# Kernel tuning notes

Hardware: AMD Instinct MI355X
Metric: run time of the kernel (lower is better)

Reference implementation:

```python
import jax, jax.numpy as jnp
import numpy as np

B, L, NV = 16, 512, 321
D, PL, ST = 128, 16, 8
P = (L - PL) // ST + 2  # 64 patches (replication pad of `stride` on the right)
E, K, H = 8, 2, 512     # experts, top-n gates, expert hidden (4*d_model)
PRED = 96
BAL_COEF, Z_COEF = 0.01, 0.001


def sinusoidal_pe(n, d):
    pos = np.arange(n)[:, None].astype(np.float32)
    div = np.exp(np.arange(0, d, 2).astype(np.float32) * -(np.log(10000.0) / d))
    pe = np.zeros((n, d), dtype=np.float32)
    pe[:, 0::2] = np.sin(pos * div)
    pe[:, 1::2] = np.cos(pos * div)
    return jnp.asarray(pe)


def setup_inputs() -> dict:
    key = jax.random.key(0)
    ks = jax.random.split(key, 12)
    s = lambda i, shape, sc: jax.random.normal(ks[i], shape, jnp.float32) * sc
    return {
        "x_enc": jax.random.normal(ks[0], (B, L, NV), jnp.float32),
        "x_mark_enc": jax.random.normal(ks[1], (B, L, 4), jnp.float32),
        "x_dec": jax.random.normal(ks[2], (B, PRED, NV), jnp.float32),
        "x_mark_dec": jax.random.normal(ks[3], (B, PRED, 4), jnp.float32),
        "W_val": s(4, (PL, D), PL ** -0.5),
        "W_g": s(5, (D, E), D ** -0.5),
        "W1": s(6, (E, D, H), D ** -0.5),
        "b1": jnp.zeros((E, H), jnp.float32),
        "W2": s(7, (E, H, D), H ** -0.5),
        "b2": jnp.zeros((E, D), jnp.float32),
        "W_head": s(8, (D * P, PRED), (D * P) ** -0.5),
        "b_head": jnp.zeros((PRED,), jnp.float32),
    }


def _forward(x_enc, W_val, W_g, W1, b1, W2, b2, W_head, b_head):
    # RevIN-style instance norm (means detached as in torch .detach())
    means = jax.lax.stop_gradient(jnp.mean(x_enc, axis=1, keepdims=True))
    xc = x_enc - means
    stdev = jnp.sqrt(jnp.var(xc, axis=1, keepdims=True) + 1e-5)
    xn = xc / stdev

    # Patch embedding: [B, NV, L] -> replicate-pad -> unfold -> linear + sinusoidal PE
    x = jnp.transpose(xn, (0, 2, 1))                        # [B, NV, L]
    x = jnp.pad(x, ((0, 0), (0, 0), (0, ST)), mode="edge")  # ReplicationPad1d((0, stride))
    idx = np.arange(P)[:, None] * ST + np.arange(PL)        # [P, PL]
    patches = x[:, :, idx]                                  # [B, NV, P, PL]
    tok = patches.reshape(B * NV, P, PL)
    emb = tok @ W_val + sinusoidal_pe(P, D)[None]           # [N, P, D]

    # MoE: top-n softmax gating (gates not renormalized), balance + router-z aux losses
    t = emb.reshape(-1, D)                                  # [T, D], T = B*NV*P
    logits = t @ W_g                                        # [T, E]
    probs = jax.nn.softmax(logits, axis=-1)
    topv, topi = jax.lax.top_k(probs, K)                    # [T, K]

    out = jnp.zeros_like(t)
    for e in range(E):  # fixed small expert count; each expert is a GELU MLP
        h = jax.nn.gelu(t @ W1[e] + b1[e], approximate=False) @ W2[e] + b2[e]
        g = jnp.sum(jnp.where(topi == e, topv, 0.0), axis=-1)  # gate for expert e (0 if unrouted)
        out = out + g[:, None] * h

    me = jnp.mean(probs, axis=0)                                            # mean router prob per expert
    ce = jnp.mean(jax.nn.one_hot(topi, E, dtype=probs.dtype).sum(1), 0) / K  # dispatch fraction per expert
    balance_loss = E * jnp.sum(me * ce)
    z_loss = jnp.mean(jax.nn.logsumexp(logits, axis=-1) ** 2)
    aux = BAL_COEF * balance_loss + Z_COEF * z_loss

    # FlattenHead: [B, NV, P, D] -> [B, NV, D, P] -> flatten(-2) -> Linear(nf, pred_len)
    enc = out.reshape(B, NV, P, D).transpose(0, 1, 3, 2)    # [B, NV, D, P]
    dec = enc.reshape(B, NV, D * P) @ W_head + b_head        # [B, NV, PRED]
    dec = jnp.transpose(dec, (0, 2, 1))                      # [B, PRED, NV]

    # de-normalize
    dec = dec * stdev[:, 0][:, None, :] + means[:, 0][:, None, :]
    return dec, aux


def reference(x_enc, x_mark_enc, x_dec, x_mark_dec, W_val, W_g, W1, b1, W2, b2, W_head, b_head):
    return _forward(x_enc, W_val, W_g, W1, b1, W2, b2, W_head, b_head)
```

## Files before the change

### kernel.cpp

```cpp
#include <hip/hip_runtime.h>
#include <hip/hip_bf16.h>

typedef unsigned short u16;
typedef unsigned int   u32;
typedef unsigned long long u64;
typedef __attribute__((ext_vector_type(8))) short bf16x8;
typedef __attribute__((ext_vector_type(4))) float f32x4;
typedef __attribute__((ext_vector_type(16))) float f32x16;
typedef __attribute__((ext_vector_type(2))) unsigned int u32x2;

#define MFMA16(a,b,c) __builtin_amdgcn_mfma_f32_16x16x32_bf16(a,b,c,0,0,0)
#define MFMA32(a,b,c) __builtin_amdgcn_mfma_f32_32x32x16_bf16(a,b,c,0,0,0)

#define NV_   321
#define B_    16
#define L_    512
#define D_    128
#define P_    64
#define E_    8
#define H_    512
#define NRW   5136
#define NTOK  328704
#define DP_   8192
#define NBUCK 329728

static __device__ __forceinline__ u16 f2bf(float f){
  __hip_bfloat16 h = __float2bfloat16(f);
  return *reinterpret_cast<u16*>(&h);
}

static __device__ __forceinline__ float gelu_f(float x){
  float x2 = x*x;
  float p  = __builtin_fmaf(-0.1029433f, x2, -2.3022083f);
  float a  = x*p;
  float en = exp2f(a);
  float r  = __builtin_amdgcn_rcpf(1.0f + en);
  return x*r;
}

static constexpr size_t alup(size_t x){ return (x + 255) & ~(size_t)255; }
static constexpr size_t OFF_MEAN = 0;
static constexpr size_t OFF_RSTD = OFF_MEAN + alup((size_t)NRW*4);
static constexpr size_t OFF_STD  = OFF_RSTD + alup((size_t)NRW*4);
static constexpr size_t OFF_XT   = OFF_STD  + alup((size_t)NRW*4);
static constexpr size_t OFF_PE   = OFF_XT   + alup((size_t)NRW*L_*4);
static constexpr size_t OFF_W1T  = OFF_PE   + alup((size_t)P_*D_*4);
static constexpr size_t OFF_W2T  = OFF_W1T  + alup((size_t)E_*H_*D_*2);
static constexpr size_t OFF_WHT  = OFF_W2T  + alup((size_t)E_*D_*H_*2);
static constexpr size_t OFF_T    = OFF_WHT  + alup((size_t)96*DP_*2);
static constexpr size_t OFF_TOPI = OFF_T    + alup((size_t)NTOK*D_*2);
static constexpr size_t OFF_GATE = OFF_TOPI + alup((size_t)NTOK*4);
static constexpr size_t OFF_CNTR = OFF_GATE + alup((size_t)NTOK*8);
static constexpr size_t OFF_BTOK = OFF_CNTR + alup((size_t)1024);
static constexpr size_t OFF_BGT  = OFF_BTOK + alup((size_t)2*NBUCK*4);
static constexpr size_t OFF_OUT  = OFF_BGT  + alup((size_t)2*NBUCK*4);
static constexpr size_t OFF_MEAND= OFF_OUT  + alup((size_t)NTOK*D_*2);
static constexpr size_t OFF_RSTDD= OFF_MEAND+ alup((size_t)NRW*8);
static constexpr size_t OFF_WVG  = OFF_RSTDD+ alup((size_t)NRW*8);
static constexpr size_t OFF_PEG  = OFF_WVG  + alup((size_t)16*8*8);
static constexpr size_t OFF_PG   = OFF_PEG  + alup((size_t)P_*E_*8);
static constexpr size_t OFF_PI   = OFF_PG   + alup((size_t)NRW*12*4);



__global__ void k_xt(const float* __restrict__ x, float* __restrict__ xT){
  __shared__ float tile[32][33];
  int b = blockIdx.z;
  int v0 = blockIdx.x*32, l0 = blockIdx.y*32;
  int tx = threadIdx.x, ty = threadIdx.y;
  for(int i=ty;i<32;i+=8){
    int l = l0+i, v = v0+tx;
    tile[i][tx] = (v<NV_) ? x[((size_t)b*L_ + l)*NV_ + v] : 0.f;
  }
  __syncthreads();
  for(int i=ty;i<32;i+=8){
    int v = v0+i, l = l0+tx;
    if(v<NV_) xT[((size_t)(b*NV_+v))*L_ + l] = tile[tx][i];
  }
}

__global__ void k_stats(const float* __restrict__ xT, float* meanp, float* rstdp, float* stdp,
                        double* meand, double* rstdd){
  __shared__ double s1[256], s2[256];
  int r = blockIdx.x, t = threadIdx.x;
  double a = (double)xT[(size_t)r*L_ + t], b = (double)xT[(size_t)r*L_ + 256 + t];
  s1[t]=a+b; s2[t]=a*a+b*b;
  __syncthreads();
  for(int o=128;o>0;o>>=1){ if(t<o){ s1[t]+=s1[t+o]; s2[t]+=s2[t+o]; } __syncthreads(); }
  if(t==0){
    double m = s1[0]*(1.0/512.0);
    double var = s2[0]*(1.0/512.0) - m*m;
    double sd = sqrt(var + 1e-5);
    meanp[r]=(float)m; stdp[r]=(float)sd; rstdp[r]=(float)(1.0/sd);
    meand[r]=m; rstdd[r]=1.0/sd;
  }
}

__global__ void k_prep(const float* __restrict__ Wval, const float* __restrict__ Wg,
                       float* __restrict__ pef, double* __restrict__ Wvg,
                       double* __restrict__ peg){
  int t = threadIdx.x;
  for(int i=t;i<8192;i+=256){
    int p = i>>7, d = i&127, k = d>>1;
    double div = exp(-(double)(2*k) * (9.210340371976184 /128.0));
    double ang = (double)p * div;
    double v = (d&1) ? cos(ang) : sin(ang);
    pef[i] = (float)v;
  }
  __syncthreads();
  if(t<128){
    int j = t>>3, e = t&7;
    double acc = 0.0;
    for(int d=0;d<128;d++) acc += (double)Wval[j*128+d] * (double)Wg[d*8+e];
    Wvg[t] = acc;
  }
  for(int q=t;q<512;q+=256){
    int p = q>>3, e = q&7;
    double acc = 0.0;
    for(int d=0;d<128;d++) acc += (double)pef[p*128+d] * (double)Wg[d*8+e];
    peg[q] = acc;
  }
}

__global__ void k_wt(const float* __restrict__ in, u16* __restrict__ outp, int R, int C){
  __shared__ float tile[32][33];
  int e = blockIdx.z;
  int c0 = blockIdx.x*32, r0 = blockIdx.y*32;
  const float* src = in + (size_t)e*R*C;
  u16* dst = outp + (size_t)e*R*C;
  int tx=threadIdx.x, ty=threadIdx.y;
  for(int i=ty;i<32;i+=8){
    int r=r0+i, c=c0+tx;
    tile[i][tx] = (r<R && c<C) ? src[(size_t)r*C+c] : 0.f;
  }
  __syncthreads();
  for(int i=ty;i<32;i+=8){
    int c=c0+i, r=r0+tx;
    if(c<C && r<R) dst[(size_t)c*R + r] = f2bf(tile[tx][i]);
  }
}

__global__ void k_wh(const float* __restrict__ Wh, u16* __restrict__ WhT2){
  __shared__ float tile[32][33];
  int d0 = blockIdx.x*32, o0 = blockIdx.y*32, p = blockIdx.z;
  int tx = threadIdx.x, ty = threadIdx.y;
  for(int i=ty;i<32;i+=8){
    int r = (d0+i)*64 + p;
    tile[i][tx] = Wh[(size_t)r*96 + o0 + tx];
  }
  __syncthreads();
  for(int i=ty;i<32;i+=8){
    int o = o0+i;
    WhT2[(size_t)o*DP_ + p*128 + d0 + tx] = f2bf(tile[tx][i]);
  }
}

__global__ __launch_bounds__(256) void k_embed(
    const float* __restrict__ xT, const float* __restrict__ meanp, const float* __restrict__ rstdp,
    const float* __restrict__ Wval, const float* __restrict__ pe,
    u16* __restrict__ tglob)
{
  __shared__ __align__(16) float xn[520];
  int r = blockIdx.x, t = threadIdx.x;
  float mean = meanp[r], rstd = rstdp[r];
  float v0 = (xT[(size_t)r*L_ + t]       - mean)*rstd;
  float v1 = (xT[(size_t)r*L_ + 256 + t] - mean)*rstd;
  xn[t] = v0; xn[t+256] = v1;
  if(t==255){
    #pragma unroll
    for(int i=512;i<520;i++) xn[i]=v1;
  }
  int d0 = (t & 63)*2;
  int p0 = t >> 6;
  float2 w[16];
  #pragma unroll
  for(int j=0;j<16;j++) w[j] = *(const float2*)(Wval + j*128 + d0);
  __syncthreads();

  for(int p=p0;p<64;p+=4){
    const float4* xp = (const float4*)(xn + p*8);
    float4 x0=xp[0], x1=xp[1], x2=xp[2], x3=xp[3];
    float xv[16];
    *(float4*)(xv+0)=x0; *(float4*)(xv+4)=x1; *(float4*)(xv+8)=x2; *(float4*)(xv+12)=x3;
    float2 pw = *(const float2*)(pe + p*128 + d0);
    float a0 = pw.x, a1 = pw.y;
    #pragma unroll
    for(int j=0;j<16;j++){ a0 += xv[j]*w[j].x; a1 += xv[j]*w[j].y; }
    u32 packed = (u32)f2bf(a0) | ((u32)f2bf(a1)<<16);
    *(u32*)(tglob + ((size_t)(r*64+p)*128 + d0)) = packed;
  }
}

__global__ __launch_bounds__(256) void k_gate(
    const float* __restrict__ xT, const double* __restrict__ meand, const double* __restrict__ rstdd,
    const double* __restrict__ Wvg, const double* __restrict__ peg,
    int* __restrict__ topip, float2* __restrict__ gatep,
    float* __restrict__ pg, int* __restrict__ pib)
{
  __shared__ double xn[520];
  __shared__ double lgt[64][9];
  int r = blockIdx.x, t = threadIdx.x;
  double m = meand[r], rs = rstdd[r];
  double v0 = ((double)xT[(size_t)r*L_ + t]       - m)*rs;
  double v1 = ((double)xT[(size_t)r*L_ + 256 + t] - m)*rs;
  xn[t]=v0; xn[t+256]=v1;
  if(t==255){
    #pragma unroll
    for(int i=512;i<520;i++) xn[i]=v1;
  }
  __syncthreads();
  for(int q=t;q<512;q+=256){
    int p = q>>3, e = q&7;
    double acc = peg[q];
    #pragma unroll
    for(int j=0;j<16;j++) acc += xn[p*8+j]*Wvg[j*8+e];
    lgt[p][e] = acc;
  }
  __syncthreads();
  if(t<64){
    int token = r*64 + t;
    double l0[8];
    #pragma unroll
    for(int e=0;e<8;e++) l0[e]=lgt[t][e];
    double mx=l0[0];
    #pragma unroll
    for(int e=1;e<8;e++) mx = fmax(mx,l0[e]);
    int i1=0; double b1v=l0[0];
    #pragma unroll
    for(int e=1;e<8;e++) if(l0[e]>b1v){b1v=l0[e]; i1=e;}
    int i2=-1; double b2v=-1e300;
    #pragma unroll
    for(int e=0;e<8;e++) if(e!=i1 && l0[e]>b2v){b2v=l0[e]; i2=e;}
    float pr[8]; float sum=0.f;
    #pragma unroll
    for(int e=0;e<8;e++){ pr[e]=__expf((float)(l0[e]-mx)); sum+=pr[e]; }
    float inv = 1.f/sum;
    #pragma unroll
    for(int e=0;e<8;e++) pr[e]*=inv;
    topip[token] = i1 | (i2<<8);
    gatep[token] = make_float2(pr[i1], pr[i2]);
    float lse = (float)mx + __logf(sum);
    #pragma unroll
    for(int e=0;e<8;e++){
      float v = pr[e];
      for(int o=32;o>0;o>>=1) v += __shfl_down(v,o);
      if(t==0) pg[r*12+e] = v;
    }
    {
      float z = lse*lse;
      for(int o=32;o>0;o>>=1) z += __shfl_down(z,o);
      if(t==0) pg[r*12+8] = z;
    }
    #pragma unroll
    for(int e=0;e<8;e++){
      u64 m1 = __ballot(i1==e);
      u64 m2 = __ballot(i2==e);
      if(t==0){
        pib[r*16+e]   = (int)__popcll(m1);
        pib[r*16+8+e] = (int)__popcll(m2);
      }
    }
  }
}

__global__ __launch_bounds__(256) void k_aux(const float* __restrict__ pg, const int* __restrict__ pib,
                                             int* __restrict__ ci, float* __restrict__ dout){
  __shared__ double sd[256];
  __shared__ int si[256];
  __shared__ double totd[9];
  __shared__ int toti[16];
  int t = threadIdx.x;
  double accd[9]; int acci[16];
  #pragma unroll
  for(int c=0;c<9;c++) accd[c]=0.0;
  #pragma unroll
  for(int c=0;c<16;c++) acci[c]=0;
  for(int r=t;r<NRW;r+=256){
    #pragma unroll
    for(int c=0;c<9;c++) accd[c] += (double)pg[r*12+c];
    #pragma unroll
    for(int c=0;c<16;c++) acci[c] += pib[r*16+c];
  }
  for(int c=0;c<9;c++){
    sd[t]=accd[c]; __syncthreads();
    for(int o=128;o>0;o>>=1){ if(t<o) sd[t]+=sd[t+o]; __syncthreads(); }
    if(t==0) totd[c]=sd[0];
    __syncthreads();
  }
  for(int c=0;c<16;c++){
    si[t]=acci[c]; __syncthreads();
    for(int o=128;o>0;o>>=1){ if(t<o) si[t]+=si[t+o]; __syncthreads(); }
    if(t==0) toti[c]=si[0];
    __syncthreads();
  }
  if(t==0){
    const double invN = 1.0/(double)NTOK;
    double bal = 0.0;
    int es1=0, bs1=0, es2=0, bs2=0;
    for(int e=0;e<8;e++){
      int c1 = toti[e], c2 = toti[8+e];
      bal += (totd[e]*invN) * ((double)(c1+c2) * invN * 0.5);
      ci[32+e]=es1; ci[16+e]=es1; ci[50+e]=bs1;
      ci[41+e]=es2; ci[24+e]=es2; ci[59+e]=bs2;
      es1 += c1; bs1 += (c1+127)>>7;
      es2 += c2; bs2 += (c2+127)>>7;
    }
    ci[40]=es1; ci[58]=bs1;
    ci[49]=es2; ci[67]=bs2;
    dout[493056] = (float)(0.01*8.0*bal + 0.001*(totd[8]*invN));
  }
}

__global__ __launch_bounds__(256) void k_scatter(const int* __restrict__ topip,
    const float2* __restrict__ gatep, int* __restrict__ ci,
    int* __restrict__ btok, float* __restrict__ bgt){
  __shared__ int lc[16]; __shared__ int lb[16];
  int t = threadIdx.x;
  int token = blockIdx.x*256 + t;
  if(t<16) lc[t]=0;
  __syncthreads();
  int ti = topip[token];
  float2 g = gatep[token];
  int e1 = ti & 255, e2 = (ti>>8)&255;
  int r1 = atomicAdd(&lc[e1],1);
  int r2 = atomicAdd(&lc[8+e2],1);
  __syncthreads();
  if(t<8)            lb[t] = atomicAdd(&ci[16+t],   lc[t]);
  else if(t<16)      lb[t] = atomicAdd(&ci[24+t-8], lc[t]);
  __syncthreads();
  int p1 = lb[e1]+r1, p2 = lb[8+e2]+r2;
  btok[p1] = token;         bgt[p1] = g.x;
  btok[NBUCK+p2] = token;   bgt[NBUCK+p2] = g.y;
}

__global__ __launch_bounds__(256,3) void k_expert(
    const u16* __restrict__ tglob,
    const u16* __restrict__ W1T, const u16* __restrict__ W2T,
    const float* __restrict__ b1g, const float* __restrict__ b2g,
    const int* __restrict__ ci,
    const int* __restrict__ btok, const float* __restrict__ bgt,
    u16* __restrict__ outg, int slot)
{
  __shared__ __align__(16) u16 Wb[2][9472];

  int bid = blockIdx.x, t = threadIdx.x;
  int stB = 32 + slot*9, bsB = 50 + slot*9;
  int boff = slot*NBUCK;
  if(bid >= ci[bsB+8]) return;
  int e = 0;
  #pragma unroll
  for(int k2=1;k2<8;k2++) if(bid >= ci[bsB+k2]) e = k2;
  int row0 = ci[stB+e] + (bid - ci[bsB+e])*128;
  int rend = ci[stB+e+1];

  int wid = t>>6, lane = t&63;
  int m = lane&31, hi = lane>>5;
  int rb = wid*32;

  int posA = row0 + rb + m;
  bool valA = posA < rend;
  int tokA  = valA ? btok[boff+posA] : 0;
  float gt  = valA ? bgt[boff+posA]  : 0.f;
  const u16* arow = tglob + (size_t)tokA*128 + hi*8;
  bf16x8 areg[8];
  #pragma unroll
  for(int ks=0;ks<8;ks++) areg[ks] = *(const bf16x8*)(arow + ks*16);

  int hr = t>>3, q = t&7;
  int dr = t>>1, q2 = t&1;

  {
    const u16* s1 = W1T + ((size_t)e*H_ + hr)*128 + q*16;
    u16* d1 = &Wb[0][hr*136 + q*16];
    *(uint4*)(d1)   = *(const uint4*)(s1);
    *(uint4*)(d1+8) = *(const uint4*)(s1+8);
    const u16* s2 = W2T + ((size_t)e*D_ + dr)*H_ + q2*16;
    u16* d2 = &Wb[0][4352 + dr*40 + q2*16];
    *(uint4*)(d2)   = *(const uint4*)(s2);
    *(uint4*)(d2+8) = *(const uint4*)(s2+8);
  }
  __syncthreads();

  f32x16 accO[4];
  #pragma unroll
  for(int nt=0;nt<4;nt++){
    const float* bp2 = b2g + e*D_ + nt*32 + 4*hi;
    #pragma unroll
    for(int qq=0;qq<4;qq++){
      float4 b4 = *(const float4*)(bp2 + 8*qq);
      accO[nt][4*qq+0]=b4.x; accO[nt][4*qq+1]=b4.y;
      accO[nt][4*qq+2]=b4.z; accO[nt][4*qq+3]=b4.w;
    }
  }

  for(int hc=0;hc<16;hc++){
    const u16* W1c = &Wb[hc&1][0];
    const u16* W2c = &Wb[hc&1][4352];
    uint4 l0,l1,l2,l3;
    if(hc<15){
      const u16* s1 = W1T + ((size_t)e*H_ + (hc+1)*32 + hr)*128 + q*16;
      l0 = *(const uint4*)(s1); l1 = *(const uint4*)(s1+8);
      const u16* s2 = W2T + ((size_t)e*D_ + dr)*H_ + (hc+1)*32 + q2*16;
      l2 = *(const uint4*)(s2); l3 = *(const uint4*)(s2+8);
    }
    f32x16 acc1;
    {
      const float* bp1 = b1g + e*H_ + hc*32 + 4*hi;
      #pragma unroll
      for(int qq=0;qq<4;qq++){
        float4 b4 = *(const float4*)(bp1 + 8*qq);
        acc1[4*qq+0]=b4.x; acc1[4*qq+1]=b4.y;
        acc1[4*qq+2]=b4.z; acc1[4*qq+3]=b4.w;
      }
    }
    #pragma unroll
    for(int ks=0;ks<8;ks++){
      bf16x8 wa = *(const bf16x8*)(W1c + m*136 + ks*16 + hi*8);
      acc1 = MFMA32(wa, areg[ks], acc1);
    }
    u32 pk[8];
    #pragma unroll
    for(int i=0;i<8;i++){
      float g0 = gelu_f(acc1[2*i]);
      float g1 = gelu_f(acc1[2*i+1]);
      asm("v_cvt_pk_bf16_f32 %0, %1, %2" : "=v"(pk[i]) : "v"(g0), "v"(g1));
    }
    union { bf16x8 v; u32 w[4]; } bA, bB;
    u32x2 s02 = __builtin_amdgcn_permlane32_swap(pk[0], pk[2], false, false);
    u32x2 s13 = __builtin_amdgcn_permlane32_swap(pk[1], pk[3], false, false);
    u32x2 s46 = __builtin_amdgcn_permlane32_swap(pk[4], pk[6], false, false);
    u32x2 s57 = __builtin_amdgcn_permlane32_swap(pk[5], pk[7], false, false);
    bA.w[0]=s02.x; bA.w[1]=s13.x; bA.w[2]=s02.y; bA.w[3]=s13.y;
    bB.w[0]=s46.x; bB.w[1]=s57.x; bB.w[2]=s46.y; bB.w[3]=s57.y;
    #pragma unroll
    for(int nt=0;nt<4;nt++){
      bf16x8 a2 = *(const bf16x8*)(W2c + (nt*32+m)*40 + hi*8);
      accO[nt] = MFMA32(a2, bA.v, accO[nt]);
    }
    #pragma unroll
    for(int nt=0;nt<4;nt++){
      bf16x8 a2 = *(const bf16x8*)(W2c + (nt*32+m)*40 + 16 + hi*8);
      accO[nt] = MFMA32(a2, bB.v, accO[nt]);
    }
    if(hc<15){
      u16* d1 = &Wb[(hc+1)&1][hr*136 + q*16];
      *(uint4*)(d1)   = l0; *(uint4*)(d1+8) = l1;
      u16* d2 = &Wb[(hc+1)&1][4352 + dr*40 + q2*16];
      *(uint4*)(d2)   = l2; *(uint4*)(d2+8) = l3;
      __syncthreads();
    }
  }

  if(valA){
    u16* obase = outg + (size_t)tokA*128 + 4*hi;
    #pragma unroll
    for(int nt=0;nt<4;nt++){
      #pragma unroll
      for(int qq=0;qq<4;qq++){
        float v0 = accO[nt][4*qq+0]*gt;
        float v1 = accO[nt][4*qq+1]*gt;
        float v2 = accO[nt][4*qq+2]*gt;
        float v3 = accO[nt][4*qq+3]*gt;
        u32* dp = (u32*)(obase + nt*32 + 8*qq);
        if(slot==1){
          u32x2 old = *(const u32x2*)dp;
          v0 += __uint_as_float(old.x<<16);
          v1 += __uint_as_float(old.x & 0xffff0000u);
          v2 += __uint_as_float(old.y<<16);
          v3 += __uint_as_float(old.y & 0xffff0000u);
        }
        u32 w0, w1;
        asm("v_cvt_pk_bf16_f32 %0, %1, %2" : "=v"(w0) : "v"(v0), "v"(v1));
        asm("v_cvt_pk_bf16_f32 %0, %1, %2" : "=v"(w1) : "v"(v2), "v"(v3));
        u32x2 nv; nv.x = w0; nv.y = w1;
        *(u32x2*)dp = nv;
      }
    }
  }
}

__global__ __launch_bounds__(256) void k_head(const u16* __restrict__ Aout,
    const u16* __restrict__ WhT2, float* __restrict__ dec8){
  int bid = blockIdx.x;
  int mb = bid>>3, kseg = bid&7;
  int t = threadIdx.x, wid = t>>6, lane = t&63;
  int quad = lane>>4, li = lane&15;
  int r0 = mb*64 + wid*16;
  int rowA = r0 + li; if(rowA >= NRW) rowA = NRW-1;
  const u16* aptr = Aout + (size_t)rowA*DP_ + kseg*1024 + quad*8;
  const u16* bptr = WhT2 + (size_t)li*DP_  + kseg*1024 + quad*8;
  f32x4 acc[6];
  #pragma unroll
  for(int j=0;j<6;j++) acc[j]=(f32x4){0,0,0,0};
  #pragma unroll 4
  for(int ks=0;ks<32;ks++){
    bf16x8 af = *(const bf16x8*)(aptr + ks*32);
    #pragma unroll
    for(int nt=0;nt<6;nt++){
      bf16x8 bw = *(const bf16x8*)(bptr + (size_t)nt*16*DP_ + ks*32);
      acc[nt] = MFMA16(af, bw, acc[nt]);
    }
  }
  float* dst = dec8 + (size_t)kseg*NRW*96;
  #pragma unroll
  for(int nt=0;nt<6;nt++)
    #pragma unroll
    for(int rg=0;rg<4;rg++){
      int mm = r0 + quad*4 + rg;
      if(mm < NRW) dst[(size_t)mm*96 + nt*16 + li] = acc[nt][rg];
    }
}

__global__ void k_final(const float* __restrict__ dec8, const float* __restrict__ bhead,
    const float* __restrict__ stdp, const float* __restrict__ meanp, float* __restrict__ outp){
  __shared__ float s[64*97];
  int b = blockIdx.y, v0 = blockIdx.x*64;
  int t = threadIdx.x;
  for(int i=t;i<6144;i+=256){
    int vi = i/96, o = i - vi*96;
    int v = v0+vi;
    float acc = 0.f;
    if(v<NV_){
      size_t base = (size_t)(b*NV_+v)*96 + o;
      #pragma unroll
      for(int ks=0;ks<8;ks++) acc += dec8[(size_t)ks*NRW*96 + base];
    }
    s[vi*97+o] = acc;
  }
  __syncthreads();
  for(int i=t;i<6144;i+=256){
    int o = i>>6, vi = i&63;
    int v = v0+vi;
    if(v<NV_){
      int r = b*NV_+v;
      outp[((size_t)b*96 + o)*NV_ + v] = (s[vi*97+o] + bhead[o])*stdp[r] + meanp[r];
    }
  }
}

extern "C" void kernel_launch(void* const* d_in, const int* in_sizes, int n_in,
                              void* d_out, int out_size, void* d_ws, size_t ws_size,
                              hipStream_t stream){
  const float* x_enc = (const float*)d_in[0];
  const float* W_val = (const float*)d_in[4];
  const float* W_g   = (const float*)d_in[5];
  const float* W1    = (const float*)d_in[6];
  const float* b1    = (const float*)d_in[7];
  const float* W2    = (const float*)d_in[8];
  const float* b2    = (const float*)d_in[9];
  const float* W_head= (const float*)d_in[10];
  const float* b_head= (const float*)d_in[11];
  float* outp = (float*)d_out;
  char* ws = (char*)d_ws;

  float* meanp = (float*)(ws+OFF_MEAN);
  float* rstdp = (float*)(ws+OFF_RSTD);
  float* stdp  = (float*)(ws+OFF_STD);
  float* xT    = (float*)(ws+OFF_XT);
  float* pe    = (float*)(ws+OFF_PE);
  u16*   W1T   = (u16*)(ws+OFF_W1T);
  u16*   W2T   = (u16*)(ws+OFF_W2T);
  u16*   WhT2  = (u16*)(ws+OFF_WHT);
  u16*   tglob = (u16*)(ws+OFF_T);
  float* dec8  = (float*)(ws+OFF_T);
  int*   topip = (int*)(ws+OFF_TOPI);
  float2* gatep= (float2*)(ws+OFF_GATE);
  int*   ci    = (int*)(ws+OFF_CNTR+128);
  int*   btok  = (int*)(ws+OFF_BTOK);
  float* bgt   = (float*)(ws+OFF_BGT);
  u16*   outg  = (u16*)(ws+OFF_OUT);
  double* meand= (double*)(ws+OFF_MEAND);
  double* rstdd= (double*)(ws+OFF_RSTDD);
  double* Wvg  = (double*)(ws+OFF_WVG);
  double* peg  = (double*)(ws+OFF_PEG);
  float* pg    = (float*)(ws+OFF_PG);
  int*   pib   = (int*)(ws+OFF_PI);

  hipMemsetAsync(ws+OFF_CNTR, 0, 1024, stream);

  k_xt<<<dim3(11,16,B_), dim3(32,8), 0, stream>>>(x_enc, xT);
  k_stats<<<NRW, 256, 0, stream>>>(xT, meanp, rstdp, stdp, meand, rstdd);
  k_prep<<<1, 256, 0, stream>>>(W_val, W_g, pe, Wvg, peg);
  k_wt<<<dim3(16,4,E_), dim3(32,8), 0, stream>>>(W1, W1T, 128, 512);
  k_wt<<<dim3(4,16,E_), dim3(32,8), 0, stream>>>(W2, W2T, 512, 128);
  k_wh<<<dim3(4,3,64), dim3(32,8), 0, stream>>>(W_head, WhT2);
  k_embed<<<NRW, 256, 0, stream>>>(xT, meanp, rstdp, W_val, pe, tglob);
  k_gate<<<NRW, 256, 0, stream>>>(xT, meand, rstdd, Wvg, peg, topip, gatep, pg, pib);
  k_aux<<<1, 256, 0, stream>>>(pg, pib, ci, outp);
  k_scatter<<<NTOK/256, 256, 0, stream>>>(topip, gatep, ci, btok, bgt);
  k_expert<<<2576, 256, 0, stream>>>(tglob, W1T, W2T, b1, b2, ci, btok, bgt, outg, 0);
  k_expert<<<2576, 256, 0, stream>>>(tglob, W1T, W2T, b1, b2, ci, btok, bgt, outg, 1);
  k_head<<<648, 256, 0, stream>>>(outg, WhT2, dec8);
  k_final<<<dim3(6,B_), 256, 0, stream>>>(dec8, b_head, stdp, meanp, outp);
}
```

Before: 641.0 us.

## Software-pipeline expert MLP: overlap GEMM2 of previous chunk with GEMM1 of current

Restructures the expert FFN loop so the second GEMM for hidden chunk hc-1 is interleaved with the first GEMM for chunk hc, while the GELU/pack of the current chunk runs after the MFMAs. W1 and W2 get separate double-buffered LDS arrays, b1 is staged once into LDS, and s_setprio is raised around the MFMA bursts. The aim is to hide GELU VALU work and LDS latency behind matrix instructions, at the cost of extra LDS, a prologue and epilogue, and more live registers that may pressure occupancy.

Result: no change. 632.6 us (-1.3%).

```diff
diff --git a/kernel.cpp b/kernel.cpp
--- a/kernel.cpp
+++ b/kernel.cpp
@@ -333,6 +333,35 @@
   btok[NBUCK+p2] = token;   bgt[NBUCK+p2] = g.y;
 }
 
+static __device__ __forceinline__ f32x16 acc1_init(const float* b1l, int hc, int hi){
+  f32x16 a;
+  const float* bp = b1l + hc*32 + 4*hi;
+  #pragma unroll
+  for(int qq=0;qq<4;qq++){
+    f32x4 b4 = *(const f32x4*)(bp + 8*qq);
+    a[4*qq+0]=b4.x; a[4*qq+1]=b4.y; a[4*qq+2]=b4.z; a[4*qq+3]=b4.w;
+  }
+  return a;
+}
+
+static __device__ __forceinline__ void gelu_pack(const f32x16& acc1, bf16x8& fA, bf16x8& fB){
+  u32 pk[8];
+  #pragma unroll
+  for(int i=0;i<8;i++){
+    float g0 = gelu_f(acc1[2*i]);
+    float g1 = gelu_f(acc1[2*i+1]);
+    asm("v_cvt_pk_bf16_f32 %0, %1, %2" : "=v"(pk[i]) : "v"(g0), "v"(g1));
+  }
+  union { bf16x8 v; u32 w[4]; } uA, uB;
+  u32x2 s02 = __builtin_amdgcn_permlane32_swap(pk[0], pk[2], false, false);
+  u32x2 s13 = __builtin_amdgcn_permlane32_swap(pk[1], pk[3], false, false);
+  u32x2 s46 = __builtin_amdgcn_permlane32_swap(pk[4], pk[6], false, false);
+  u32x2 s57 = __builtin_amdgcn_permlane32_swap(pk[5], pk[7], false, false);
+  uA.w[0]=s02.x; uA.w[1]=s13.x; uA.w[2]=s02.y; uA.w[3]=s13.y;
+  uB.w[0]=s46.x; uB.w[1]=s57.x; uB.w[2]=s46.y; uB.w[3]=s57.y;
+  fA = uA.v; fB = uB.v;
+}
+
 __global__ __launch_bounds__(256,3) void k_expert(
     const u16* __restrict__ tglob,
     const u16* __restrict__ W1T, const u16* __restrict__ W2T,
@@ -341,7 +370,9 @@
     const int* __restrict__ btok, const float* __restrict__ bgt,
     u16* __restrict__ outg, int slot)
 {
-  __shared__ __align__(16) u16 Wb[2][9472];
+  __shared__ __align__(16) u16 W1b[2][4352];
+  __shared__ __align__(16) u16 W2b[2][5120];
+  __shared__ __align__(16) float b1l[512];
 
   int bid = blockIdx.x, t = threadIdx.x;
   int stB = 32 + slot*9, bsB = 50 + slot*9;
@@ -356,6 +387,22 @@
   int wid = t>>6, lane = t&63;
   int m = lane&31, hi = lane>>5;
   int rb = wid*32;
+
+  int hr = t>>3, q = t&7;
+  int dr = t>>1, q2 = t&1;
+
+  {
+    const u16* s1 = W1T + ((size_t)e*H_ + hr)*128 + q*16;
+    uint4 p0 = *(const uint4*)(s1);
+    uint4 p1 = *(const uint4*)(s1+8);
+    u16* d1 = &W1b[0][hr*136 + q*16];
+    *(uint4*)(d1)   = p0;
+    *(uint4*)(d1+8) = p1;
+    if(t<128){
+      float4 bv = *(const float4*)(b1g + e*H_ + t*4);
+      *(float4*)(b1l + t*4) = bv;
+    }
+  }
 
   int posA = row0 + rb + m;
   bool valA = posA < rend;
@@ -366,21 +413,6 @@
   #pragma unroll
   for(int ks=0;ks<8;ks++) areg[ks] = *(const bf16x8*)(arow + ks*16);
 
-  int hr = t>>3, q = t&7;
-  int dr = t>>1, q2 = t&1;
-
-  {
-    const u16* s1 = W1T + ((size_t)e*H_ + hr)*128 + q*16;
-    u16* d1 = &Wb[0][hr*136 + q*16];
-    *(uint4*)(d1)   = *(const uint4*)(s1);
-    *(uint4*)(d1+8) = *(const uint4*)(s1+8);
-    const u16* s2 = W2T + ((size_t)e*D_ + dr)*H_ + q2*16;
-    u16* d2 = &Wb[0][4352 + dr*40 + q2*16];
-    *(uint4*)(d2)   = *(const uint4*)(s2);
-    *(uint4*)(d2+8) = *(const uint4*)(s2+8);
-  }
-  __syncthreads();
-
   f32x16 accO[4];
   #pragma unroll
   for(int nt=0;nt<4;nt++){
@@ -392,63 +424,67 @@
       accO[nt][4*qq+2]=b4.z; accO[nt][4*qq+3]=b4.w;
     }
   }
-
-  for(int hc=0;hc<16;hc++){
-    const u16* W1c = &Wb[hc&1][0];
-    const u16* W2c = &Wb[hc&1][4352];
-    uint4 l0,l1,l2,l3;
+  __syncthreads();
+
+  bf16x8 fA, fB;
+  {
+    const u16* s1 = W1T + ((size_t)e*H_ + 32 + hr)*128 + q*16;
+    uint4 l0 = *(const uint4*)(s1), l1 = *(const uint4*)(s1+8);
+    const u16* s2 = W2T + ((size_t)e*D_ + dr)*H_ + q2*16;
+    uint4 l2 = *(const uint4*)(s2), l3 = *(const uint4*)(s2+8);
+    f32x16 acc1 = acc1_init(b1l, 0, hi);
+    __builtin_amdgcn_s_setprio(1);
+    #pragma unroll
+    for(int ks=0;ks<8;ks++){
+      bf16x8 wa = *(const bf16x8*)(&W1b[0][0] + m*136 + ks*16 + hi*8);
+      acc1 = MFMA32(wa, areg[ks], acc1);
+    }
+    __builtin_amdgcn_s_setprio(0);
+    u16* d1 = &W1b[1][hr*136 + q*16];
+    *(uint4*)(d1)   = l0; *(uint4*)(d1+8) = l1;
+    u16* d2 = &W2b[0][dr*40 + q2*16];
+    *(uint4*)(d2)   = l2; *(uint4*)(d2+8) = l3;
+    gelu_pack(acc1, fA, fB);
+    __syncthreads();
+  }
+  for(int hc=1; hc<16; hc++){
+    uint4 l0, l1;
     if(hc<15){
       const u16* s1 = W1T + ((size_t)e*H_ + (hc+1)*32 + hr)*128 + q*16;
       l0 = *(const uint4*)(s1); l1 = *(const uint4*)(s1+8);
-      const u16* s2 = W2T + ((size_t)e*D_ + dr)*H_ + (hc+1)*32 + q2*16;
-      l2 = *(const uint4*)(s2); l3 = *(const uint4*)(s2+8);
-    }
-    f32x16 acc1;
-    {
-      const float* bp1 = b1g + e*H_ + hc*32 + 4*hi;
-      #pragma unroll
-      for(int qq=0;qq<4;qq++){
-        float4 b4 = *(const float4*)(bp1 + 8*qq);
-        acc1[4*qq+0]=b4.x; acc1[4*qq+1]=b4.y;
-        acc1[4*qq+2]=b4.z; acc1[4*qq+3]=b4.w;
-      }
-    }
+    }
+    const u16* s2 = W2T + ((size_t)e*D_ + dr)*H_ + hc*32 + q2*16;
+    uint4 l2 = *(const uint4*)(s2), l3 = *(const uint4*)(s2+8);
+    f32x16 acc1 = acc1_init(b1l, hc, hi);
+    const u16* W1c = &W1b[hc&1][0];
+    const u16* W2p = &W2b[(hc-1)&1][0];
+    __builtin_amdgcn_s_setprio(1);
     #pragma unroll
     for(int ks=0;ks<8;ks++){
       bf16x8 wa = *(const bf16x8*)(W1c + m*136 + ks*16 + hi*8);
       acc1 = MFMA32(wa, areg[ks], acc1);
-    }
-    u32 pk[8];
-    #pragma unroll
-    for(int i=0;i<8;i++){
-      float g0 = gelu_f(acc1[2*i]);
-      float g1 = gelu_f(acc1[2*i+1]);
-      asm("v_cvt_pk_bf16_f32 %0, %1, %2" : "=v"(pk[i]) : "v"(g0), "v"(g1));
-    }
-    union { bf16x8 v; u32 w[4]; } bA, bB;
-    u32x2 s02 = __builtin_amdgcn_permlane32_swap(pk[0], pk[2], false, false);
-    u32x2 s13 = __builtin_amdgcn_permlane32_swap(pk[1], pk[3], false, false);
-    u32x2 s46 = __builtin_amdgcn_permlane32_swap(pk[4], pk[6], false, false);
-    u32x2 s57 = __builtin_amdgcn_permlane32_swap(pk[5], pk[7], false, false);
-    bA.w[0]=s02.x; bA.w[1]=s13.x; bA.w[2]=s02.y; bA.w[3]=s13.y;
-    bB.w[0]=s46.x; bB.w[1]=s57.x; bB.w[2]=s46.y; bB.w[3]=s57.y;
-    #pragma unroll
-    for(int nt=0;nt<4;nt++){
-      bf16x8 a2 = *(const bf16x8*)(W2c + (nt*32+m)*40 + hi*8);
-      accO[nt] = MFMA32(a2, bA.v, accO[nt]);
-    }
-    #pragma unroll
-    for(int nt=0;nt<4;nt++){
-      bf16x8 a2 = *(const bf16x8*)(W2c + (nt*32+m)*40 + 16 + hi*8);
-      accO[nt] = MFMA32(a2, bB.v, accO[nt]);
-    }
+      bf16x8 a2 = *(const bf16x8*)(W2p + ((ks&3)*32+m)*40 + (ks>>2)*16 + hi*8);
+      accO[ks&3] = MFMA32(a2, (ks>>2)?fB:fA, accO[ks&3]);
+    }
+    __builtin_amdgcn_s_setprio(0);
     if(hc<15){
-      u16* d1 = &Wb[(hc+1)&1][hr*136 + q*16];
+      u16* d1 = &W1b[(hc+1)&1][hr*136 + q*16];
       *(uint4*)(d1)   = l0; *(uint4*)(d1+8) = l1;
-      u16* d2 = &Wb[(hc+1)&1][4352 + dr*40 + q2*16];
-      *(uint4*)(d2)   = l2; *(uint4*)(d2+8) = l3;
-      __syncthreads();
-    }
+    }
+    u16* d2 = &W2b[hc&1][dr*40 + q2*16];
+    *(uint4*)(d2)   = l2; *(uint4*)(d2+8) = l3;
+    gelu_pack(acc1, fA, fB);
+    __syncthreads();
+  }
+  {
+    const u16* W2p = &W2b[1][0];
+    __builtin_amdgcn_s_setprio(1);
+    #pragma unroll
+    for(int ks=0;ks<8;ks++){
+      bf16x8 a2 = *(const bf16x8*)(W2p + ((ks&3)*32+m)*40 + (ks>>2)*16 + hi*8);
+      accO[ks&3] = MFMA32(a2, (ks>>2)?fB:fA, accO[ks&3]);
+    }
+    __builtin_amdgcn_s_setprio(0);
   }
 
   if(valA){
```
